# Optimization experiments

Hardware: AMD Instinct MI355X
Metric: run time of the kernel (lower is better)

The kernel has to match this reference:

```python
import jax, jax.numpy as jnp
import numpy as np

DIM = 1024
HEADS = 8
NUM_KEYS = 256
TOPK = 32
D_HEAD = DIM // HEADS
BATCH = 2
SEQ = 2048


def setup_inputs() -> dict:
    key = jax.random.key(0)
    ks = jax.random.split(key, 5)
    x = jax.random.normal(ks[0], (BATCH, SEQ, DIM), jnp.float32)
    # nn.Linear(dim, 2*dim, bias=False): weight (2*dim, dim)
    Wq = jax.random.normal(ks[1], (2 * DIM, DIM), jnp.float32) * (DIM ** -0.5)
    # nn.Parameter(torch.randn(heads, num_keys, 2, d_head))
    keys = jax.random.normal(ks[2], (HEADS, NUM_KEYS, 2, D_HEAD), jnp.float32)
    # nn.Parameter(torch.randn(heads, num_keys**2, d_head))
    values = jax.random.normal(ks[3], (HEADS, NUM_KEYS ** 2, D_HEAD), jnp.float32)
    # nn.Linear(dim, dim): weight (dim, dim), bias (dim,)
    Wo = jax.random.normal(ks[4], (DIM, DIM), jnp.float32) * (DIM ** -0.5)
    bo = jnp.zeros((DIM,), jnp.float32)
    return {"x": x, "Wq": Wq, "keys": keys, "values": values, "Wo": Wo, "bo": bo}


def reference(x, Wq, keys, values, Wo, bo):
    b, t, e = x.shape
    h, dh, k, nk = HEADS, D_HEAD, TOPK, NUM_KEYS
    # to_queries + chunk(2, dim=-1) + stack -> (2, b, t, h, d_head)
    q = x @ Wq.T                                    # (b, t, 2*dim)
    q = q.reshape(b, t, 2, e).transpose(2, 0, 1, 3)  # (2, b, t, dim), matches chunk+stack
    q = q.reshape(2, b, t, h, dh)
    # dual sub-key scores: (b, h, t, 2, num_keys)
    dots = jnp.einsum('pbthd,hnpd->bhtpn', q, keys)
    # top-k over num_keys per sub-key
    scores, indices = jax.lax.top_k(dots, k)         # (b, h, t, 2, k)
    # faithful to source: chunk(2, dim=2) splits the TIME axis
    th = t // 2
    s0, s1 = scores[:, :, :th], scores[:, :, th:]
    i0, i1 = indices[:, :, :th], indices[:, :, th:]
    # Cartesian combination: (b, h, t//2, 2, k, k) -> (b, h, t, k*k)
    all_scores = (s0[..., :, None] + s1[..., None, :]).reshape(b, h, t, k * k)
    all_indices = (i0[..., :, None] * nk + i1[..., None, :]).reshape(b, h, t, k * k)
    # final top-k over the k^2 candidates
    final_scores, final_idx = jax.lax.top_k(all_scores, k)   # (b, h, t, k)
    value_indices = jnp.take_along_axis(all_indices, final_idx, axis=-1)  # (b, h, t, k)
    attn = jax.nn.softmax(final_scores, axis=-1)
    # gather values per head: values (h, nk^2, dh), idx (b, h, t, k) -> (b, h, t, k, dh)
    sel = jax.vmap(lambda v, idx: v[idx], in_axes=(0, 1), out_axes=1)(values, value_indices)
    out = jnp.einsum('bhtk,bhtkd->bhtd', attn, sel)  # weighted sum over top-k
    out = out.transpose(0, 2, 1, 3).reshape(b, t, e)
    return out @ Wo.T + bo
```

## Files before the change

### kernel.cpp

```cpp
#include <hip/hip_runtime.h>

typedef unsigned int u32;
typedef unsigned long long u64;
typedef _Float16 f16;
typedef __attribute__((ext_vector_type(8))) _Float16 f16x8;
typedef __attribute__((ext_vector_type(4))) float f32x4;

#define TSEQ 2048
#define PAD 40

__device__ __forceinline__ u32 f2sort(float f) {
  u32 u = __float_as_uint(f);
  return u ^ ((u32)((int)u >> 31) | 0x80000000u);
}
__device__ __forceinline__ float sort2f(u32 u) {
  u ^= (u & 0x80000000u) ? 0x80000000u : 0xFFFFFFFFu;
  return __uint_as_float(u);
}

__device__ __forceinline__ f16x8 cvt8(float4 a, float4 b) {
  f16x8 r;
  r[0] = (f16)a.x; r[1] = (f16)a.y; r[2] = (f16)a.z; r[3] = (f16)a.w;
  r[4] = (f16)b.x; r[5] = (f16)b.y; r[6] = (f16)b.z; r[7] = (f16)b.w;
  return r;
}

__global__ __launch_bounds__(256) void gemm_mfma_nt(
    const float* __restrict__ A, int lda,
    const float* __restrict__ B, int ldb,
    const float* __restrict__ bias,
    float* __restrict__ C, int ldc, int K, int dots) {
  if (dots) {
    int z = blockIdx.z;
    int h = z >> 1, p = z & 1;
    A += p * 1024 + h * 128;
    B += (size_t)(h * 512 + p) * 128;
    C += (size_t)z * 4096 * 256;
  }
  __shared__ f16 As[128 * PAD];
  __shared__ f16 Bs[128 * PAD];
  const int tid = threadIdx.x;
  const int m0 = blockIdx.y << 7, n0 = blockIdx.x << 7;
  const int srow = tid >> 1;
  const int sk = (tid & 1) << 4;
  const float* Ap = A + (size_t)(m0 + srow) * lda + sk;
  const float* Bp = B + (size_t)(n0 + srow) * ldb + sk;
  const int lane = tid & 63;
  const int wave = tid >> 6;
  const int wm = (wave >> 1) << 6;
  const int wn = (wave & 1) << 6;
  const int fm = lane & 15;
  const int fk = (lane >> 4) << 3;
  f32x4 acc[4][4] = {};
  for (int k0 = 0; k0 < K; k0 += 32) {
    float4 av0 = *(const float4*)(Ap + k0);
    float4 av1 = *(const float4*)(Ap + k0 + 4);
    float4 av2 = *(const float4*)(Ap + k0 + 8);
    float4 av3 = *(const float4*)(Ap + k0 + 12);
    float4 bv0 = *(const float4*)(Bp + k0);
    float4 bv1 = *(const float4*)(Bp + k0 + 4);
    float4 bv2 = *(const float4*)(Bp + k0 + 8);
    float4 bv3 = *(const float4*)(Bp + k0 + 12);
    __syncthreads();
    *(f16x8*)&As[srow * PAD + sk] = cvt8(av0, av1);
    *(f16x8*)&As[srow * PAD + sk + 8] = cvt8(av2, av3);
    *(f16x8*)&Bs[srow * PAD + sk] = cvt8(bv0, bv1);
    *(f16x8*)&Bs[srow * PAD + sk + 8] = cvt8(bv2, bv3);
    __syncthreads();
    f16x8 af[4], bf[4];
#pragma unroll
    for (int mi = 0; mi < 4; mi++)
      af[mi] = *(const f16x8*)&As[(wm + mi * 16 + fm) * PAD + fk];
#pragma unroll
    for (int nj = 0; nj < 4; nj++)
      bf[nj] = *(const f16x8*)&Bs[(wn + nj * 16 + fm) * PAD + fk];
#pragma unroll
    for (int mi = 0; mi < 4; mi++)
#pragma unroll
      for (int nj = 0; nj < 4; nj++)
        acc[mi][nj] = __builtin_amdgcn_mfma_f32_16x16x32_f16(
            af[mi], bf[nj], acc[mi][nj], 0, 0, 0);
  }
  float bb[4];
#pragma unroll
  for (int nj = 0; nj < 4; nj++)
    bb[nj] = bias ? bias[n0 + wn + nj * 16 + fm] : 0.f;
#pragma unroll
  for (int mi = 0; mi < 4; mi++) {
#pragma unroll
    for (int r = 0; r < 4; r++) {
      int row = m0 + wm + mi * 16 + ((lane >> 4) << 2) + r;
      float* cp = C + (size_t)row * ldc + n0 + wn + fm;
#pragma unroll
      for (int nj = 0; nj < 4; nj++) cp[nj * 16] = acc[mi][nj][r] + bb[nj];
    }
  }
}

__global__ __launch_bounds__(256) void topk1(
    const float* __restrict__ D, float* __restrict__ s1score,
    int* __restrict__ s1idx) {
  const int tid = threadIdx.x;
  const int rloc = tid >> 4;
  const int l = tid & 15;
  const int wid = blockIdx.x * 16 + rloc;
  const float* row = D + (size_t)wid * 256;
  u32 key[16];
#pragma unroll
  for (int s = 0; s < 16; s++) {
    float v = row[l + 16 * s];
    key[s] = (f2sort(v) & ~0xFFu) | (u32)s;
  }
  const int wl = tid & 63;
  const int grp = wl & 48;
  float myw0 = 0.f, myw1 = 0.f;
  int myi0 = 0, myi1 = 0;
  for (int it = 0; it < 32; it++) {
    u32 lm = key[0];
#pragma unroll
    for (int s = 1; s < 16; s++) lm = key[s] > lm ? key[s] : lm;
    u32 gm = lm;
#pragma unroll
    for (int d = 1; d < 16; d <<= 1) {
      u32 o = (u32)__shfl_xor((int)gm, d);
      gm = o > gm ? o : gm;
    }
    u64 mask = __ballot(lm == gm);
    int owner = __ffsll((u64)((mask >> grp) & 0xFFFFull)) - 1;
    int swin = (int)(gm & 0xFFu);
    int idx = swin * 16 + owner;
    float score = sort2f(gm & ~0xFFu);
    bool isown = (l == owner);
#pragma unroll
    for (int s = 0; s < 16; s++)
      key[s] = (isown && s == swin) ? 0u : key[s];
    if (l == (it & 15)) {
      if (it < 16) { myw0 = score; myi0 = idx; }
      else         { myw1 = score; myi1 = idx; }
    }
  }
  int hp = wid >> 12, r = wid & 4095;
  int h = hp >> 1, p = hp & 1;
  int b = r >> 11, t = r & 2047;
  size_t orow = ((((size_t)(b * 8 + h)) * TSEQ + t) * 2 + p) * 32;
  s1score[orow + l] = myw0;
  s1score[orow + l + 16] = myw1;
  s1idx[orow + l] = myi0;
  s1idx[orow + l + 16] = myi1;
}

__global__ __launch_bounds__(256) void topk2_gather(
    const float* __restrict__ s1s, const int* __restrict__ s1i,
    const float* __restrict__ values, float* __restrict__ headout) {
  __shared__ unsigned short cand[128];
  __shared__ float s0sh[16][32];
  __shared__ float s1sh[16][32];
  __shared__ int i0sh[16][32];
  __shared__ int i1sh[16][32];
  const int tid = threadIdx.x;
  if (tid < 128) {
    int c = tid;
    unsigned short enc = 0xFFFF;
    if (c < 119) {
      int rem = c, i = 0;
      for (i = 0; i < 32; i++) {
        int cnt = 32 / (i + 1);
        if (rem < cnt) break;
        rem -= cnt;
      }
      enc = (unsigned short)((i << 5) | rem);
    }
    cand[tid] = enc;
  }
  const int rloc = tid >> 4;
  const int l = tid & 15;
  const int row = blockIdx.x * 16 + rloc;
  const int b = row >> 14;
  const int h = (row >> 11) & 7;
  const int t = row & 2047;
  const int tt = t >> 1, p = t & 1;
  size_t rbase = (size_t)(b * 8 + h) * TSEQ;
  size_t base0 = ((rbase + tt) * 2 + p) * 32;
  size_t base1 = ((rbase + tt + 1024) * 2 + p) * 32;
  s0sh[rloc][l] = s1s[base0 + l];
  s0sh[rloc][l + 16] = s1s[base0 + l + 16];
  s1sh[rloc][l] = s1s[base1 + l];
  s1sh[rloc][l + 16] = s1s[base1 + l + 16];
  i0sh[rloc][l] = s1i[base0 + l];
  i0sh[rloc][l + 16] = s1i[base0 + l + 16];
  i1sh[rloc][l] = s1i[base1 + l];
  i1sh[rloc][l + 16] = s1i[base1 + l + 16];
  __syncthreads();
  u32 key[8];
#pragma unroll
  for (int s = 0; s < 8; s++) {
    int c = l + 16 * s;
    unsigned short e = cand[c];
    u32 kk = 0u;
    if (e != 0xFFFF) {
      float v = s0sh[rloc][e >> 5] + s1sh[rloc][e & 31];
      kk = (f2sort(v) & ~0xFFu) | (u32)s;
    }
    key[s] = kk;
  }
  const int wl = tid & 63;
  const int grp = wl & 48;
  float myw0 = 0.f, myw1 = 0.f;
  int myv0 = 0, myv1 = 0;
  for (int it = 0; it < 32; it++) {
    u32 lm = key[0];
#pragma unroll
    for (int s = 1; s < 8; s++) lm = key[s] > lm ? key[s] : lm;
    u32 gm = lm;
#pragma unroll
    for (int d = 1; d < 16; d <<= 1) {
      u32 o = (u32)__shfl_xor((int)gm, d);
      gm = o > gm ? o : gm;
    }
    u64 mask = __ballot(lm == gm);
    int owner = __ffsll((u64)((mask >> grp) & 0xFFFFull)) - 1;
    int swin = (int)(gm & 0xFFu);
    unsigned short e = cand[owner + 16 * swin];
    int wi = e >> 5, wj = e & 31;
    float score = sort2f(gm & ~0xFFu);
    int vidx = i0sh[rloc][wi] * 256 + i1sh[rloc][wj];
    bool isown = (l == owner);
#pragma unroll
    for (int s = 0; s < 8; s++)
      key[s] = (isown && s == swin) ? 0u : key[s];
    if (l == (it & 15)) {
      if (it < 16) { myw0 = score; myv0 = vidx; }
      else         { myw1 = score; myv1 = vidx; }
    }
  }
  float m0 = __shfl(myw0, grp);
  float e0 = __expf(myw0 - m0);
  float e1 = __expf(myw1 - m0);
  float ssum = e0 + e1;
#pragma unroll
  for (int d = 1; d < 16; d <<= 1) ssum += __shfl_xor(ssum, d);
  float inv = 1.0f / ssum;
  float a0 = e0 * inv, a1 = e1 * inv;
  const float* vb = values + (((size_t)h) << 16) * 128 + l * 8;
  float4 acc0 = make_float4(0.f, 0.f, 0.f, 0.f);
  float4 acc1 = make_float4(0.f, 0.f, 0.f, 0.f);
#pragma unroll 8
  for (int k = 0; k < 32; k++) {
    int src = grp + (k & 15);
    int vi = __shfl((k < 16) ? myv0 : myv1, src);
    float wk = __shfl((k < 16) ? a0 : a1, src);
    const float* vp = vb + (size_t)vi * 128;
    float4 x0 = *(const float4*)(vp);
    float4 x1 = *(const float4*)(vp + 4);
    acc0.x += wk * x0.x; acc0.y += wk * x0.y;
    acc0.z += wk * x0.z; acc0.w += wk * x0.w;
    acc1.x += wk * x1.x; acc1.y += wk * x1.y;
    acc1.z += wk * x1.z; acc1.w += wk * x1.w;
  }
  float* op = headout + (size_t)(b * TSEQ + t) * 1024 + h * 128 + l * 8;
  *(float4*)(op) = acc0;
  *(float4*)(op + 4) = acc1;
}

extern "C" void kernel_launch(void* const* d_in, const int* in_sizes, int n_in,
                              void* d_out, int out_size, void* d_ws,
                              size_t ws_size, hipStream_t stream) {
  const float* x    = (const float*)d_in[0];
  const float* Wq   = (const float*)d_in[1];
  const float* keys = (const float*)d_in[2];
  const float* vals = (const float*)d_in[3];
  const float* Wo   = (const float*)d_in[4];
  const float* bo   = (const float*)d_in[5];
  float* out = (float*)d_out;
  char* ws = (char*)d_ws;
  float* Q    = (float*)(ws);
  float* Dbuf = (float*)(ws + (size_t)(32u << 20));
  float* s1s  = (float*)(ws + (size_t)(96u << 20));
  int*   s1i  = (int*)(ws + (size_t)(104u << 20));
  float* headout = (float*)(ws);

  gemm_mfma_nt<<<dim3(16, 32, 1), 256, 0, stream>>>(x, 1024, Wq, 1024, nullptr,
                                                    Q, 2048, 1024, 0);
  gemm_mfma_nt<<<dim3(2, 32, 16), 256, 0, stream>>>(Q, 2048, keys, 256,
                                                    nullptr, Dbuf, 256, 128, 1);
  topk1<<<dim3(65536 / 16), 256, 0, stream>>>(Dbuf, s1s, s1i);
  topk2_gather<<<dim3(32768 / 16), 256, 0, stream>>>(s1s, s1i, vals, headout);
  gemm_mfma_nt<<<dim3(8, 32, 1), 256, 0, stream>>>(headout, 1024, Wo, 1024, bo,
                                                   out, 1024, 1024, 0);
}
```

Before: 593.3 us.

## Pre-convert inputs to f16, fuse dots with first top-k, use direct-to-LDS loads

A single up-front kernel converts x, Wq, Wo and keys to f16. The GEMMs then stream f16 tiles straight into LDS with global_load_lds instead of loading fp32 and converting per tile. The sub-key dot products are fused with the first top-k, so the fp32 score matrix is never written out and read back. Q and the head outputs are stored as f16, which halves intermediate traffic. In exchange the conversion pass adds an extra kernel, the unpadded LDS layout may cause bank conflicts, and the fused top-k kernel launches only 1024 blocks.

```diff
diff --git a/kernel.cpp b/kernel.cpp
--- a/kernel.cpp
+++ b/kernel.cpp
@@ -3,11 +3,13 @@
 typedef unsigned int u32;
 typedef unsigned long long u64;
 typedef _Float16 f16;
+typedef __attribute__((ext_vector_type(4))) _Float16 f16x4;
 typedef __attribute__((ext_vector_type(8))) _Float16 f16x8;
 typedef __attribute__((ext_vector_type(4))) float f32x4;
+typedef const __attribute__((address_space(1))) void* gp_t;
+typedef __attribute__((address_space(3))) void* lp_t;
 
 #define TSEQ 2048
-#define PAD 40
 
 __device__ __forceinline__ u32 f2sort(float f) {
   u32 u = __float_as_uint(f);
@@ -18,62 +20,60 @@
   return __uint_as_float(u);
 }
 
-__device__ __forceinline__ f16x8 cvt8(float4 a, float4 b) {
-  f16x8 r;
-  r[0] = (f16)a.x; r[1] = (f16)a.y; r[2] = (f16)a.z; r[3] = (f16)a.w;
-  r[4] = (f16)b.x; r[5] = (f16)b.y; r[6] = (f16)b.z; r[7] = (f16)b.w;
-  return r;
-}
-
-__global__ __launch_bounds__(256) void gemm_mfma_nt(
-    const float* __restrict__ A, int lda,
-    const float* __restrict__ B, int ldb,
-    const float* __restrict__ bias,
-    float* __restrict__ C, int ldc, int K, int dots) {
-  if (dots) {
-    int z = blockIdx.z;
-    int h = z >> 1, p = z & 1;
-    A += p * 1024 + h * 128;
-    B += (size_t)(h * 512 + p) * 128;
-    C += (size_t)z * 4096 * 256;
-  }
-  __shared__ f16 As[128 * PAD];
-  __shared__ f16 Bs[128 * PAD];
+__device__ __forceinline__ void glds16(const f16* g, f16* l) {
+  __builtin_amdgcn_global_load_lds((gp_t)g, (lp_t)l, 16, 0, 0);
+}
+
+__global__ __launch_bounds__(256) void cvt_all(
+    const float* __restrict__ x, const float* __restrict__ wq,
+    const float* __restrict__ wo, const float* __restrict__ ky,
+    f16* __restrict__ xd, f16* __restrict__ wqd, f16* __restrict__ wod,
+    f16* __restrict__ kyd) {
+  int g = blockIdx.x * 256 + threadIdx.x;
+  const float* s;
+  f16* d;
+  int off;
+  if (g < 1048576)      { s = x;  d = xd;  off = g; }
+  else if (g < 1572864) { s = wq; d = wqd; off = g - 1048576; }
+  else if (g < 1835008) { s = wo; d = wod; off = g - 1572864; }
+  else                  { s = ky; d = kyd; off = g - 1835008; }
+  float4 v = ((const float4*)s)[off];
+  f16x4 o;
+  o[0] = (f16)v.x; o[1] = (f16)v.y; o[2] = (f16)v.z; o[3] = (f16)v.w;
+  ((f16x4*)d)[off] = o;
+}
+
+__global__ __launch_bounds__(256) void gemm_f16(
+    const f16* __restrict__ A, int lda, const f16* __restrict__ B, int ldb,
+    const float* __restrict__ bias, void* __restrict__ Cv, int ldc, int K,
+    int c_f16) {
+  __shared__ f16 As[128 * 32];
+  __shared__ f16 Bs[128 * 32];
   const int tid = threadIdx.x;
+  const int lane = tid & 63, wave = tid >> 6;
   const int m0 = blockIdx.y << 7, n0 = blockIdx.x << 7;
-  const int srow = tid >> 1;
-  const int sk = (tid & 1) << 4;
-  const float* Ap = A + (size_t)(m0 + srow) * lda + sk;
-  const float* Bp = B + (size_t)(n0 + srow) * ldb + sk;
-  const int lane = tid & 63;
-  const int wave = tid >> 6;
-  const int wm = (wave >> 1) << 6;
-  const int wn = (wave & 1) << 6;
-  const int fm = lane & 15;
-  const int fk = (lane >> 4) << 3;
+  const int c0 = wave * 128 + lane, c1 = c0 + 64;
+  const int r0 = c0 >> 2, s0 = c0 & 3;
+  const int r1 = c1 >> 2, s1 = c1 & 3;
+  const f16* Ab = A + (size_t)m0 * lda;
+  const f16* Bb = B + (size_t)n0 * ldb;
+  const int fm = lane & 15, fq = lane >> 4, fk = fq << 3;
+  const int wm = (wave >> 1) << 6, wn = (wave & 1) << 6;
   f32x4 acc[4][4] = {};
   for (int k0 = 0; k0 < K; k0 += 32) {
-    float4 av0 = *(const float4*)(Ap + k0);
-    float4 av1 = *(const float4*)(Ap + k0 + 4);
-    float4 av2 = *(const float4*)(Ap + k0 + 8);
-    float4 av3 = *(const float4*)(Ap + k0 + 12);
-    float4 bv0 = *(const float4*)(Bp + k0);
-    float4 bv1 = *(const float4*)(Bp + k0 + 4);
-    float4 bv2 = *(const float4*)(Bp + k0 + 8);
-    float4 bv3 = *(const float4*)(Bp + k0 + 12);
     __syncthreads();
-    *(f16x8*)&As[srow * PAD + sk] = cvt8(av0, av1);
-    *(f16x8*)&As[srow * PAD + sk + 8] = cvt8(av2, av3);
-    *(f16x8*)&Bs[srow * PAD + sk] = cvt8(bv0, bv1);
-    *(f16x8*)&Bs[srow * PAD + sk + 8] = cvt8(bv2, bv3);
+    glds16(Ab + (size_t)r0 * lda + k0 + s0 * 8, As + (size_t)c0 * 8 - lane * 8);
+    glds16(Ab + (size_t)r1 * lda + k0 + s1 * 8, As + (size_t)c1 * 8 - lane * 8);
+    glds16(Bb + (size_t)r0 * ldb + k0 + s0 * 8, Bs + (size_t)c0 * 8 - lane * 8);
+    glds16(Bb + (size_t)r1 * ldb + k0 + s1 * 8, Bs + (size_t)c1 * 8 - lane * 8);
     __syncthreads();
     f16x8 af[4], bf[4];
 #pragma unroll
     for (int mi = 0; mi < 4; mi++)
-      af[mi] = *(const f16x8*)&As[(wm + mi * 16 + fm) * PAD + fk];
+      af[mi] = *(const f16x8*)&As[(wm + mi * 16 + fm) * 32 + fk];
 #pragma unroll
     for (int nj = 0; nj < 4; nj++)
-      bf[nj] = *(const f16x8*)&Bs[(wn + nj * 16 + fm) * PAD + fk];
+      bf[nj] = *(const f16x8*)&Bs[(wn + nj * 16 + fm) * 32 + fk];
 #pragma unroll
     for (int mi = 0; mi < 4; mi++)
 #pragma unroll
@@ -81,77 +81,115 @@
         acc[mi][nj] = __builtin_amdgcn_mfma_f32_16x16x32_f16(
             af[mi], bf[nj], acc[mi][nj], 0, 0, 0);
   }
-  float bb[4];
-#pragma unroll
-  for (int nj = 0; nj < 4; nj++)
-    bb[nj] = bias ? bias[n0 + wn + nj * 16 + fm] : 0.f;
-#pragma unroll
-  for (int mi = 0; mi < 4; mi++) {
-#pragma unroll
-    for (int r = 0; r < 4; r++) {
-      int row = m0 + wm + mi * 16 + ((lane >> 4) << 2) + r;
-      float* cp = C + (size_t)row * ldc + n0 + wn + fm;
-#pragma unroll
-      for (int nj = 0; nj < 4; nj++) cp[nj * 16] = acc[mi][nj][r] + bb[nj];
-    }
-  }
-}
-
-__global__ __launch_bounds__(256) void topk1(
-    const float* __restrict__ D, float* __restrict__ s1score,
-    int* __restrict__ s1idx) {
+  if (c_f16) {
+    f16* C = (f16*)Cv;
+#pragma unroll
+    for (int mi = 0; mi < 4; mi++)
+#pragma unroll
+      for (int r = 0; r < 4; r++) {
+        int row = m0 + wm + mi * 16 + fq * 4 + r;
+        f16* cp = C + (size_t)row * ldc + n0 + wn + fm;
+#pragma unroll
+        for (int nj = 0; nj < 4; nj++) cp[nj * 16] = (f16)acc[mi][nj][r];
+      }
+  } else {
+    float* C = (float*)Cv;
+    float bb[4];
+#pragma unroll
+    for (int nj = 0; nj < 4; nj++)
+      bb[nj] = bias ? bias[n0 + wn + nj * 16 + fm] : 0.f;
+#pragma unroll
+    for (int mi = 0; mi < 4; mi++)
+#pragma unroll
+      for (int r = 0; r < 4; r++) {
+        int row = m0 + wm + mi * 16 + fq * 4 + r;
+        float* cp = C + (size_t)row * ldc + n0 + wn + fm;
+#pragma unroll
+        for (int nj = 0; nj < 4; nj++) cp[nj * 16] = acc[mi][nj][r] + bb[nj];
+      }
+  }
+}
+
+__global__ __launch_bounds__(256) void dots_topk1(
+    const f16* __restrict__ Q,
+    const f16* __restrict__ keysf,
+    float* __restrict__ s1s, int* __restrict__ s1i) {
+  __shared__ f16 As[64 * 32];
+  __shared__ f16 Bs[256 * 32];
   const int tid = threadIdx.x;
-  const int rloc = tid >> 4;
-  const int l = tid & 15;
-  const int wid = blockIdx.x * 16 + rloc;
-  const float* row = D + (size_t)wid * 256;
-  u32 key[16];
-#pragma unroll
-  for (int s = 0; s < 16; s++) {
-    float v = row[l + 16 * s];
-    key[s] = (f2sort(v) & ~0xFFu) | (u32)s;
-  }
-  const int wl = tid & 63;
-  const int grp = wl & 48;
-  float myw0 = 0.f, myw1 = 0.f;
-  int myi0 = 0, myi1 = 0;
-  for (int it = 0; it < 32; it++) {
-    u32 lm = key[0];
-#pragma unroll
-    for (int s = 1; s < 16; s++) lm = key[s] > lm ? key[s] : lm;
-    u32 gm = lm;
-#pragma unroll
-    for (int d = 1; d < 16; d <<= 1) {
-      u32 o = (u32)__shfl_xor((int)gm, d);
-      gm = o > gm ? o : gm;
-    }
-    u64 mask = __ballot(lm == gm);
-    int owner = __ffsll((u64)((mask >> grp) & 0xFFFFull)) - 1;
-    int swin = (int)(gm & 0xFFu);
-    int idx = swin * 16 + owner;
-    float score = sort2f(gm & ~0xFFu);
-    bool isown = (l == owner);
-#pragma unroll
-    for (int s = 0; s < 16; s++)
-      key[s] = (isown && s == swin) ? 0u : key[s];
-    if (l == (it & 15)) {
-      if (it < 16) { myw0 = score; myi0 = idx; }
-      else         { myw1 = score; myi1 = idx; }
-    }
-  }
-  int hp = wid >> 12, r = wid & 4095;
-  int h = hp >> 1, p = hp & 1;
-  int b = r >> 11, t = r & 2047;
-  size_t orow = ((((size_t)(b * 8 + h)) * TSEQ + t) * 2 + p) * 32;
-  s1score[orow + l] = myw0;
-  s1score[orow + l + 16] = myw1;
-  s1idx[orow + l] = myi0;
-  s1idx[orow + l + 16] = myi1;
+  const int lane = tid & 63, wave = tid >> 6;
+  const int z = blockIdx.y;
+  const int h = z >> 1, p = z & 1;
+  const int m0 = blockIdx.x << 6;
+  const f16* Aq = Q + (size_t)m0 * 2048 + p * 1024 + h * 128;
+  const f16* Bk = keysf + ((size_t)h * 512 + p) * 128;
+  const int cA = wave * 64 + lane;
+  const int rA = cA >> 2, sA = cA & 3;
+  const int fm = lane & 15, fq = lane >> 4, fk = fq << 3;
+  f32x4 acc[16] = {};
+  for (int k0 = 0; k0 < 128; k0 += 32) {
+    __syncthreads();
+    glds16(Aq + (size_t)rA * 2048 + k0 + sA * 8, As + (size_t)cA * 8 - lane * 8);
+#pragma unroll
+    for (int c = 0; c < 4; c++) {
+      int cB = (wave * 4 + c) * 64 + lane;
+      int rB = cB >> 2, sB = cB & 3;
+      glds16(Bk + (size_t)rB * 256 + k0 + sB * 8,
+             Bs + (size_t)cB * 8 - lane * 8);
+    }
+    __syncthreads();
+    f16x8 af = *(const f16x8*)&As[(wave * 16 + fm) * 32 + fk];
+#pragma unroll
+    for (int j = 0; j < 16; j++) {
+      f16x8 bf = *(const f16x8*)&Bs[(j * 16 + fm) * 32 + fk];
+      acc[j] = __builtin_amdgcn_mfma_f32_16x16x32_f16(af, bf, acc[j], 0, 0, 0);
+    }
+  }
+  const int grp = lane & 48;
+  for (int r = 0; r < 4; r++) {
+    u32 key[16];
+#pragma unroll
+    for (int j = 0; j < 16; j++)
+      key[j] = (f2sort(acc[j][r]) & ~0xFFu) | (u32)j;
+    float myw0 = 0.f, myw1 = 0.f;
+    int myi0 = 0, myi1 = 0;
+    for (int it = 0; it < 32; it++) {
+      u32 lm = key[0];
+#pragma unroll
+      for (int j = 1; j < 16; j++) lm = key[j] > lm ? key[j] : lm;
+      u32 gm = lm;
+#pragma unroll
+      for (int d = 1; d < 16; d <<= 1) {
+        u32 o = (u32)__shfl_xor((int)gm, d);
+        gm = o > gm ? o : gm;
+      }
+      u64 mask = __ballot(lm == gm);
+      int owner = __ffsll((u64)((mask >> grp) & 0xFFFFull)) - 1;
+      int swin = (int)(gm & 0xFFu);
+      int idx = swin * 16 + owner;
+      float score = sort2f(gm & ~0xFFu);
+      bool isown = (fm == owner);
+#pragma unroll
+      for (int j = 0; j < 16; j++)
+        key[j] = (isown && j == swin) ? 0u : key[j];
+      if (fm == (it & 15)) {
+        if (it < 16) { myw0 = score; myi0 = idx; }
+        else         { myw1 = score; myi1 = idx; }
+      }
+    }
+    int m = m0 + wave * 16 + (fq << 2) + r;
+    int b = m >> 11, t = m & 2047;
+    size_t orow = ((((size_t)(b * 8 + h)) * TSEQ + t) * 2 + p) * 32;
+    s1s[orow + fm] = myw0;
+    s1s[orow + fm + 16] = myw1;
+    s1i[orow + fm] = myi0;
+    s1i[orow + fm + 16] = myi1;
+  }
 }
 
 __global__ __launch_bounds__(256) void topk2_gather(
     const float* __restrict__ s1s, const int* __restrict__ s1i,
-    const float* __restrict__ values, float* __restrict__ headout) {
+    const float* __restrict__ values, f16* __restrict__ headout) {
   __shared__ unsigned short cand[128];
   __shared__ float s0sh[16][32];
   __shared__ float s1sh[16][32];
@@ -203,8 +241,7 @@
     }
     key[s] = kk;
   }
-  const int wl = tid & 63;
-  const int grp = wl & 48;
+  const int grp = tid & 48;
   float myw0 = 0.f, myw1 = 0.f;
   int myv0 = 0, myv1 = 0;
   for (int it = 0; it < 32; it++) {
@@ -257,9 +294,11 @@
     acc1.x += wk * x1.x; acc1.y += wk * x1.y;
     acc1.z += wk * x1.z; acc1.w += wk * x1.w;
   }
-  float* op = headout + (size_t)(b * TSEQ + t) * 1024 + h * 128 + l * 8;
-  *(float4*)(op) = acc0;
-  *(float4*)(op + 4) = acc1;
+  f16x8 o;
+  o[0] = (f16)acc0.x; o[1] = (f16)acc0.y; o[2] = (f16)acc0.z; o[3] = (f16)acc0.w;
+  o[4] = (f16)acc1.x; o[5] = (f16)acc1.y; o[6] = (f16)acc1.z; o[7] = (f16)acc1.w;
+  f16* op = headout + (size_t)(b * TSEQ + t) * 1024 + h * 128 + l * 8;
+  *(f16x8*)op = o;
 }
 
 extern "C" void kernel_launch(void* const* d_in, const int* in_sizes, int n_in,
@@ -273,18 +312,20 @@
   const float* bo   = (const float*)d_in[5];
   float* out = (float*)d_out;
   char* ws = (char*)d_ws;
-  float* Q    = (float*)(ws);
-  float* Dbuf = (float*)(ws + (size_t)(32u << 20));
-  float* s1s  = (float*)(ws + (size_t)(96u << 20));
-  int*   s1i  = (int*)(ws + (size_t)(104u << 20));
-  float* headout = (float*)(ws);
-
-  gemm_mfma_nt<<<dim3(16, 32, 1), 256, 0, stream>>>(x, 1024, Wq, 1024, nullptr,
-                                                    Q, 2048, 1024, 0);
-  gemm_mfma_nt<<<dim3(2, 32, 16), 256, 0, stream>>>(Q, 2048, keys, 256,
-                                                    nullptr, Dbuf, 256, 128, 1);
-  topk1<<<dim3(65536 / 16), 256, 0, stream>>>(Dbuf, s1s, s1i);
-  topk2_gather<<<dim3(32768 / 16), 256, 0, stream>>>(s1s, s1i, vals, headout);
-  gemm_mfma_nt<<<dim3(8, 32, 1), 256, 0, stream>>>(headout, 1024, Wo, 1024, bo,
-                                                   out, 1024, 1024, 0);
-}
+  f16*   xf  = (f16*)(ws);
+  f16*   wqf = (f16*)(ws + (size_t)(8u << 20));
+  f16*   wof = (f16*)(ws + (size_t)(12u << 20));
+  f16*   kyf = (f16*)(ws + (size_t)(14u << 20));
+  f16*   Qf  = (f16*)(ws + (size_t)(16u << 20));
+  float* s1s = (float*)(ws + (size_t)(32u << 20));
+  int*   s1i = (int*)(ws + (size_t)(40u << 20));
+  f16*   hof = (f16*)(ws + (size_t)(48u << 20));
+
+  cvt_all<<<dim3(7680), 256, 0, stream>>>(x, Wq, Wo, keys, xf, wqf, wof, kyf);
+  gemm_f16<<<dim3(16, 32), 256, 0, stream>>>(xf, 1024, wqf, 1024, nullptr, Qf,
+                                             2048, 1024, 1);
+  dots_topk1<<<dim3(64, 16), 256, 0, stream>>>(Qf, kyf, s1s, s1i);
+  topk2_gather<<<dim3(32768 / 16), 256, 0, stream>>>(s1s, s1i, vals, hof);
+  gemm_f16<<<dim3(8, 32), 256, 0, stream>>>(hof, 1024, wof, 1024, bo, out,
+                                            1024, 1024, 0);
+}
```

New measurement: 570.3 us. -3.9%, faster.
